# Kernel optimization log

Measured on AMD Instinct MI355X. Metric: run time of the kernel, lower is better.

The kernel has to match this reference:

```python
import jax, jax.numpy as jnp
import numpy as np
from jax import lax

BATCH, N_RES, N_BINS, N_FRAMES = 16, 8, 256, 2048
INIT_W = 0.04


def setup_inputs() -> dict:
    key = jax.random.key(0)
    k1, k2 = jax.random.split(key)
    inp = jax.random.uniform(k1, (BATCH, N_RES, N_BINS, N_FRAMES), dtype=jnp.float32)
    initial_state = jax.random.uniform(k2, (BATCH, N_RES, N_BINS), dtype=jnp.float32)
    weight = jnp.full((N_RES, N_BINS), INIT_W, dtype=jnp.float32)  # per-filter smoothing coeff
    return {"input": inp, "initial_state": initial_state, "weight": weight}


def reference(input, initial_state, weight):
    # clamp_constraint(w, 0, 1), then broadcast (n_res, n_bins) -> (1, n_res, n_bins)
    w = jnp.clip(weight, 0.0, 1.0)[None, :, :]
    one_minus_w = 1.0 - w
    # scan over the frame axis: y[n] = w*x[n] + (1-w)*y[n-1], y[-1] = initial_state
    xs = jnp.moveaxis(input, -1, 0)  # (n_frames, batch, n_res, n_bins)

    def step(y_prev, x):
        y = w * x + one_minus_w * y_prev
        return y, y

    _, ys = lax.scan(step, initial_state, xs)
    return jnp.moveaxis(ys, 0, -1)  # (batch, n_res, n_bins, n_frames)
```

## Files before the change

### kernel.cpp

```cpp
#include <hip/hip_runtime.h>


#define N_FRAMES 2048
#define FRAMES_PER_LANE 32
#define VEC_PER_LANE 8

__global__ __launch_bounds__(64) void ema_scan_kernel(
    const float* __restrict__ x,
    const float* __restrict__ y0,
    const float* __restrict__ wgt,
    float* __restrict__ out) {
  const int s = blockIdx.x;
  const int lane = threadIdx.x;

  const float w_raw = wgt[s & 2047];
  const float w = fminf(fmaxf(w_raw, 0.0f), 1.0f);
  const float a = 1.0f - w;

  const float4* in4 =
      reinterpret_cast<const float4*>(x + (size_t)s * N_FRAMES) +
      lane * VEC_PER_LANE;
  float4 v[VEC_PER_LANE];
#pragma unroll
  for (int k = 0; k < VEC_PER_LANE; ++k) v[k] = in4[k];

  float b = 0.0f;
#pragma unroll
  for (int k = 0; k < VEC_PER_LANE; ++k) {
    b = fmaf(a, b, w * v[k].x);
    b = fmaf(a, b, w * v[k].y);
    b = fmaf(a, b, w * v[k].z);
    b = fmaf(a, b, w * v[k].w);
  }
  const float a2 = a * a;
  const float a4 = a2 * a2;
  const float a8 = a4 * a4;
  const float a16 = a8 * a8;
  const float a32 = a16 * a16;

  float Ai = a32;
  float Bi = b;
#pragma unroll
  for (int d = 1; d < 64; d <<= 1) {
    float Ap = __shfl_up(Ai, d, 64);
    float Bp = __shfl_up(Bi, d, 64);
    if (lane >= d) {
      Bi = fmaf(Ai, Bp, Bi);
      Ai = Ai * Ap;
    }
  }

  const float Ae = __shfl_up(Ai, 1, 64);
  const float Be = __shfl_up(Bi, 1, 64);
  const float ys = y0[s];
  float y = (lane == 0) ? ys : fmaf(Ae, ys, Be);

  float4* o4 = reinterpret_cast<float4*>(out + (size_t)s * N_FRAMES) +
               lane * VEC_PER_LANE;
#pragma unroll
  for (int k = 0; k < VEC_PER_LANE; ++k) {
    float4 r;
    y = fmaf(a, y, w * v[k].x); r.x = y;
    y = fmaf(a, y, w * v[k].y); r.y = y;
    y = fmaf(a, y, w * v[k].z); r.z = y;
    y = fmaf(a, y, w * v[k].w); r.w = y;
    o4[k] = r;
  }
}

extern "C" void kernel_launch(void* const* d_in, const int* in_sizes, int n_in,
                              void* d_out, int out_size, void* d_ws, size_t ws_size,
                              hipStream_t stream) {
  const float* x   = (const float*)d_in[0];
  const float* y0  = (const float*)d_in[1];
  const float* wgt = (const float*)d_in[2];
  float* out = (float*)d_out;

  const int n_seq = 16 * 8 * 256;
  ema_scan_kernel<<<dim3(n_seq), dim3(64), 0, stream>>>(x, y0, wgt, out);
}
```

Baseline: 438.5 us.

## Use coalesced interleaved chunk layout with per-chunk wave scans and carry

Each lane now takes float4 elements strided by 64 across eight chunks instead of one contiguous 32-frame span, so every load and store instruction across the wave is fully coalesced. Each chunk runs a B-only wave scan with precomputed power constants, and a serial carry links the chunks. Four sequences share a 256-thread block to cut block count. This adds eight scans' worth of shuffles in exchange for better memory access, which matters because the kernel is bandwidth bound.

```diff
diff --git a/kernel.cpp b/kernel.cpp
--- a/kernel.cpp
+++ b/kernel.cpp
@@ -2,69 +2,82 @@
 
 
 #define N_FRAMES 2048
-#define FRAMES_PER_LANE 32
-#define VEC_PER_LANE 8
+#define CHUNKS 8
+#define SEQ_PER_BLOCK 4
 
-__global__ __launch_bounds__(64) void ema_scan_kernel(
+__global__ __launch_bounds__(256) void ema_scan_kernel(
     const float* __restrict__ x,
     const float* __restrict__ y0,
     const float* __restrict__ wgt,
     float* __restrict__ out) {
-  const int s = blockIdx.x;
-  const int lane = threadIdx.x;
+  const int lane = threadIdx.x & 63;
+  const int wid  = threadIdx.x >> 6;
+  const int s = blockIdx.x * SEQ_PER_BLOCK + wid;
 
   const float w_raw = wgt[s & 2047];
   const float w = fminf(fmaxf(w_raw, 0.0f), 1.0f);
   const float a = 1.0f - w;
 
-  const float4* in4 =
-      reinterpret_cast<const float4*>(x + (size_t)s * N_FRAMES) +
-      lane * VEC_PER_LANE;
-  float4 v[VEC_PER_LANE];
+  const float a4   = (a * a) * (a * a);
+  const float A1   = a4;
+  const float A2   = A1 * A1;
+  const float A4   = A2 * A2;
+  const float A8   = A4 * A4;
+  const float A16  = A8 * A8;
+  const float A32  = A16 * A16;
+  const float a256 = A32 * A32;
+
+  float powl = 1.0f;
+  powl *= (lane & 1)  ? A1  : 1.0f;
+  powl *= (lane & 2)  ? A2  : 1.0f;
+  powl *= (lane & 4)  ? A4  : 1.0f;
+  powl *= (lane & 8)  ? A8  : 1.0f;
+  powl *= (lane & 16) ? A16 : 1.0f;
+  powl *= (lane & 32) ? A32 : 1.0f;
+
+  const float4* in4 = reinterpret_cast<const float4*>(x + (size_t)s * N_FRAMES);
+  float4*       o4  = reinterpret_cast<float4*>(out + (size_t)s * N_FRAMES);
+
+  float4 v[CHUNKS];
 #pragma unroll
-  for (int k = 0; k < VEC_PER_LANE; ++k) v[k] = in4[k];
+  for (int k = 0; k < CHUNKS; ++k) v[k] = in4[k * 64 + lane];
 
-  float b = 0.0f;
+  float b[CHUNKS];
 #pragma unroll
-  for (int k = 0; k < VEC_PER_LANE; ++k) {
-    b = fmaf(a, b, w * v[k].x);
-    b = fmaf(a, b, w * v[k].y);
-    b = fmaf(a, b, w * v[k].z);
-    b = fmaf(a, b, w * v[k].w);
-  }
-  const float a2 = a * a;
-  const float a4 = a2 * a2;
-  const float a8 = a4 * a4;
-  const float a16 = a8 * a8;
-  const float a32 = a16 * a16;
-
-  float Ai = a32;
-  float Bi = b;
-#pragma unroll
-  for (int d = 1; d < 64; d <<= 1) {
-    float Ap = __shfl_up(Ai, d, 64);
-    float Bp = __shfl_up(Bi, d, 64);
-    if (lane >= d) {
-      Bi = fmaf(Ai, Bp, Bi);
-      Ai = Ai * Ap;
-    }
+  for (int k = 0; k < CHUNKS; ++k) {
+    float t = w * v[k].x;
+    t = fmaf(a, t, w * v[k].y);
+    t = fmaf(a, t, w * v[k].z);
+    t = fmaf(a, t, w * v[k].w);
+    b[k] = t;
   }
 
-  const float Ae = __shfl_up(Ai, 1, 64);
-  const float Be = __shfl_up(Bi, 1, 64);
-  const float ys = y0[s];
-  float y = (lane == 0) ? ys : fmaf(Ae, ys, Be);
+#pragma unroll
+  for (int k = 0; k < CHUNKS; ++k) {
+    float t = b[k];
+    float p;
+    p = __shfl_up(t, 1, 64);  if (lane >= 1)  t = fmaf(A1,  p, t);
+    p = __shfl_up(t, 2, 64);  if (lane >= 2)  t = fmaf(A2,  p, t);
+    p = __shfl_up(t, 4, 64);  if (lane >= 4)  t = fmaf(A4,  p, t);
+    p = __shfl_up(t, 8, 64);  if (lane >= 8)  t = fmaf(A8,  p, t);
+    p = __shfl_up(t, 16, 64); if (lane >= 16) t = fmaf(A16, p, t);
+    p = __shfl_up(t, 32, 64); if (lane >= 32) t = fmaf(A32, p, t);
+    b[k] = t;
+  }
 
-  float4* o4 = reinterpret_cast<float4*>(out + (size_t)s * N_FRAMES) +
-               lane * VEC_PER_LANE;
+  float carry = y0[s];
 #pragma unroll
-  for (int k = 0; k < VEC_PER_LANE; ++k) {
+  for (int k = 0; k < CHUNKS; ++k) {
+    float excl = __shfl_up(b[k], 1, 64);
+    if (lane == 0) excl = 0.0f;
+    float y = fmaf(powl, carry, excl);
     float4 r;
     y = fmaf(a, y, w * v[k].x); r.x = y;
     y = fmaf(a, y, w * v[k].y); r.y = y;
     y = fmaf(a, y, w * v[k].z); r.z = y;
     y = fmaf(a, y, w * v[k].w); r.w = y;
-    o4[k] = r;
+    o4[k * 64 + lane] = r;
+    carry = fmaf(a256, carry, __shfl(b[k], 63, 64));
   }
 }
 
@@ -77,5 +90,5 @@
   float* out = (float*)d_out;
 
   const int n_seq = 16 * 8 * 256;
-  ema_scan_kernel<<<dim3(n_seq), dim3(64), 0, stream>>>(x, y0, wgt, out);
+  ema_scan_kernel<<<dim3(n_seq / SEQ_PER_BLOCK), dim3(256), 0, stream>>>(x, y0, wgt, out);
 }
```

Result: no change. 431.1 us (-1.7%).
